# Optimization experiments

Measured on AMD Instinct MI355X. Metric: run time of the kernel, lower is better.

Reference implementation:

```python
import jax, jax.numpy as jnp
import numpy as np

EMBED_DIM = 1024
NUM_HEADS = 16
HEAD_DIM = EMBED_DIM // NUM_HEADS
BOARD = 32
SEQ = BOARD * BOARD
BATCH = 16


def setup_inputs() -> dict:
    key = jax.random.key(0)
    ks = jax.random.split(key, 6)
    x = jax.random.normal(ks[0], (BATCH, SEQ, EMBED_DIM), dtype=jnp.float32)
    scale = 1.0 / np.sqrt(EMBED_DIM)
    Wq = jax.random.normal(ks[1], (EMBED_DIM, EMBED_DIM), dtype=jnp.float32) * scale
    Wk = jax.random.normal(ks[2], (EMBED_DIM, EMBED_DIM), dtype=jnp.float32) * scale
    Wv = jax.random.normal(ks[3], (EMBED_DIM, EMBED_DIM), dtype=jnp.float32) * scale
    Wo = jax.random.normal(ks[4], (EMBED_DIM, EMBED_DIM), dtype=jnp.float32) * scale
    rel_bias = jax.random.normal(ks[5], (NUM_HEADS, 2 * BOARD - 1), dtype=jnp.float32)
    return {"x": x, "Wq": Wq, "Wk": Wk, "Wv": Wv, "Wo": Wo, "rel_bias": rel_bias}


def _rel_indices():
    # coords of the flattened H*W grid
    idx = jnp.arange(SEQ)
    rows = idx // BOARD
    cols = idx % BOARD
    offset = BOARD - 1
    rel_x = cols[None, :] - cols[:, None] + offset  # [S, S]
    rel_y = rows[None, :] - rows[:, None] + offset  # [S, S]
    return rel_x, rel_y


def reference(x, Wq, Wk, Wv, Wo, rel_bias):
    B, S, E = x.shape
    H, D = NUM_HEADS, HEAD_DIM
    # projections (Linear with bias=False: x @ W.T; weights here stored as [E, E] applied as x @ W)
    q = (x @ Wq).reshape(B, S, H, D).transpose(0, 2, 1, 3)  # [B,H,S,D]
    k = (x @ Wk).reshape(B, S, H, D).transpose(0, 2, 1, 3)
    v = (x @ Wv).reshape(B, S, H, D).transpose(0, 2, 1, 3)
    scores = jnp.einsum('bhqd,bhkd->bhqk', q, k) / jnp.sqrt(jnp.float32(D))
    rel_x, rel_y = _rel_indices()
    bias = rel_bias[:, rel_x] + rel_bias[:, rel_y]  # [H, S, S]
    scores = scores + bias[None]
    attn = jax.nn.softmax(scores, axis=-1)
    out = jnp.einsum('bhqk,bhkd->bhqd', attn, v)
    out = out.transpose(0, 2, 1, 3).reshape(B, S, E)
    return out @ Wo
```

## Files before the change

### kernel.cpp

```cpp
#include <hip/hip_runtime.h>

#define SEQ   1024
#define EMBED 1024
#define NH    16
#define HD    64
#define NB    16

typedef float facc4 __attribute__((ext_vector_type(4)));
typedef float facc16 __attribute__((ext_vector_type(16)));
typedef short frag8 __attribute__((ext_vector_type(8)));
typedef short sv4 __attribute__((ext_vector_type(4)));

__device__ __forceinline__ unsigned short f2bf(float f) {
  union { float f; unsigned int u; } c; c.f = f;
  unsigned int u = c.u;
  u += 0x7FFFu + ((u >> 16) & 1u);
  return (unsigned short)(u >> 16);
}

__device__ __forceinline__ unsigned int pk_bf16(float lo, float hi) {
  unsigned int r;
  asm("v_cvt_pk_bf16_f32 %0, %1, %2" : "=v"(r) : "v"(lo), "v"(hi));
  return r;
}

__device__ __forceinline__ void gl_lds16(const void* g, void* l) {
  __builtin_amdgcn_global_load_lds(
      (const __attribute__((address_space(1))) unsigned int*)g,
      (__attribute__((address_space(3))) unsigned int*)l, 16, 0, 0);
}

__global__ __launch_bounds__(256) void convert_x_kernel(
    const float* __restrict__ x, unsigned short* __restrict__ xb, int n8) {
  int stride = gridDim.x * blockDim.x;
  for (int i = blockIdx.x * blockDim.x + threadIdx.x; i < n8; i += stride) {
    const float4* src = (const float4*)(x + (size_t)i * 8);
    float4 v0 = src[0], v1 = src[1];
    frag8 o;
    o[0] = f2bf(v0.x); o[1] = f2bf(v0.y); o[2] = f2bf(v0.z); o[3] = f2bf(v0.w);
    o[4] = f2bf(v1.x); o[5] = f2bf(v1.y); o[6] = f2bf(v1.z); o[7] = f2bf(v1.w);
    *(frag8*)(xb + (size_t)i * 8) = o;
  }
}

__global__ __launch_bounds__(256) void transpose_w_kernel(
    const float* W0, const float* W1, const float* W2, const float* W3,
    unsigned short* T0, unsigned short* T1, unsigned short* T2, unsigned short* T3) {
  __shared__ float tw[64][65];
  const float* W; unsigned short* T;
  switch (blockIdx.z) {
    case 0: W = W0; T = T0; break;
    case 1: W = W1; T = T1; break;
    case 2: W = W2; T = T2; break;
    default: W = W3; T = T3; break;
  }
  int k0 = blockIdx.y * 64, n0 = blockIdx.x * 64;
  int t = threadIdx.x;
#pragma unroll
  for (int rep = 0; rep < 4; ++rep) {
    int c = rep * 256 + t;
    int row = c >> 4, ch = c & 15;
    float4 v = *(const float4*)(W + (size_t)(k0 + row) * 1024 + n0 + ch * 4);
    tw[row][ch * 4 + 0] = v.x; tw[row][ch * 4 + 1] = v.y;
    tw[row][ch * 4 + 2] = v.z; tw[row][ch * 4 + 3] = v.w;
  }
  __syncthreads();
#pragma unroll
  for (int rep = 0; rep < 2; ++rep) {
    int c = rep * 256 + t;
    int nrow = c >> 3, ch = c & 7;
    frag8 o;
#pragma unroll
    for (int i = 0; i < 8; ++i) o[i] = (short)f2bf(tw[ch * 8 + i][nrow]);
    *(frag8*)(T + (size_t)(n0 + nrow) * 1024 + k0 + ch * 8) = o;
  }
}

template <int MODE>
__global__ __launch_bounds__(512, 2) void gemm256(
    const unsigned short* __restrict__ A, const unsigned short* __restrict__ Bt,
    unsigned short* __restrict__ qo, unsigned short* __restrict__ ko,
    unsigned short* __restrict__ vto, float* __restrict__ fo, int N) {
  __shared__ unsigned short a_s[2][256 * 64];
  __shared__ unsigned short b_s[2][256 * 64];
  const int tid = threadIdx.x;
  const int w = tid >> 6, l = tid & 63;
  const int l15 = l & 15, l4 = l >> 4;
  const int wr = w >> 2, wc = w & 3;

  const int bid = blockIdx.x;
  const int xcd = bid & 7, j = bid >> 3;
  const int mt = xcd * 8 + (j & 7), nt = j >> 3;
  const int m0 = mt << 8, n0 = nt << 8;

  const int ldrow = l >> 3;
  const int swz8 = ((l & 7) ^ (ldrow & 7)) << 3;
  const unsigned short* Ab = A + (size_t)m0 * 1024;
  const unsigned short* Bb = Bt + (size_t)n0 * 1024;

  facc4 acc[8][4];
#pragma unroll
  for (int mi = 0; mi < 8; ++mi)
#pragma unroll
    for (int nj = 0; nj < 4; ++nj)
#pragma unroll
      for (int r = 0; r < 4; ++r) acc[mi][nj][r] = 0.f;

  auto STAGE = [&](int buf, int kt) {
#pragma unroll
    for (int i = 0; i < 4; ++i) {
      const int c = (w << 2) + i;
      gl_lds16(Ab + (size_t)kt * 64 + (size_t)((c << 3) + ldrow) * 1024 + swz8,
               &a_s[buf][c << 9]);
      gl_lds16(Bb + (size_t)kt * 64 + (size_t)((c << 3) + ldrow) * 1024 + swz8,
               &b_s[buf][c << 9]);
    }
  };

  STAGE(0, 0);
  STAGE(1, 1);
  asm volatile("s_waitcnt vmcnt(8)" ::: "memory");
  __builtin_amdgcn_s_barrier();
  __builtin_amdgcn_sched_barrier(0);

  const int rowA = (wr << 7) + l15;
  const int rowB = (wc << 6) + l15;

  for (int t = 0; t < 16; ++t) {
    const int cur = t & 1;
    const unsigned short* ap = a_s[cur];
    const unsigned short* bp = b_s[cur];
    frag8 af[8], bf[4];

#pragma unroll
    for (int mi = 0; mi < 8; ++mi) {
      const int r = rowA + (mi << 4);
      af[mi] = *(const frag8*)(ap + (r << 6) + ((l4 ^ (r & 7)) << 3));
    }
#pragma unroll
    for (int nj = 0; nj < 4; ++nj) {
      const int r = rowB + (nj << 4);
      bf[nj] = *(const frag8*)(bp + (r << 6) + ((l4 ^ (r & 7)) << 3));
    }
    __builtin_amdgcn_s_setprio(1);
#pragma unroll
    for (int mi = 0; mi < 8; ++mi)
#pragma unroll
      for (int nj = 0; nj < 4; ++nj)
        acc[mi][nj] = __builtin_amdgcn_mfma_f32_16x16x32_bf16(
            af[mi], bf[nj], acc[mi][nj], 0, 0, 0);
    __builtin_amdgcn_s_setprio(0);

    frag8 ag[8], bg[4];
#pragma unroll
    for (int mi = 0; mi < 8; ++mi) {
      const int r = rowA + (mi << 4);
      ag[mi] = *(const frag8*)(ap + (r << 6) + (((4 + l4) ^ (r & 7)) << 3));
    }
#pragma unroll
    for (int nj = 0; nj < 4; ++nj) {
      const int r = rowB + (nj << 4);
      bg[nj] = *(const frag8*)(bp + (r << 6) + (((4 + l4) ^ (r & 7)) << 3));
    }
    asm volatile("s_waitcnt lgkmcnt(0)" ::: "memory");
    __builtin_amdgcn_s_barrier();
    __builtin_amdgcn_sched_barrier(0);
    if (t + 2 < 16) STAGE(cur, t + 2);

    __builtin_amdgcn_s_setprio(1);
#pragma unroll
    for (int mi = 0; mi < 8; ++mi)
#pragma unroll
      for (int nj = 0; nj < 4; ++nj)
        acc[mi][nj] = __builtin_amdgcn_mfma_f32_16x16x32_bf16(
            ag[mi], bg[nj], acc[mi][nj], 0, 0, 0);
    __builtin_amdgcn_s_setprio(0);

    if (t < 14)       asm volatile("s_waitcnt vmcnt(8)" ::: "memory");
    else if (t == 14) asm volatile("s_waitcnt vmcnt(0)" ::: "memory");
    if (t < 15) {
      __builtin_amdgcn_s_barrier();
      __builtin_amdgcn_sched_barrier(0);
    }
  }

  const int m_base = m0 + (wr << 7);
  if (MODE == 0) {
    const int bb16 = (m_base >> 10) << 4;
#pragma unroll
    for (int nj = 0; nj < 4; ++nj) {
      const int n = n0 + (wc << 6) + (nj << 4) + l15;
      const int proj = n >> 10, rem = n & 1023;
      const int h = rem >> 6, d = rem & 63;
      const size_t bh16 = ((size_t)(bb16 + h)) << 16;
      if (proj == 2) {
#pragma unroll
        for (int mi = 0; mi < 8; ++mi) {
          const int s0 = (m_base + (mi << 4) + (l4 << 2)) & 1023;
          sv4 pv;
#pragma unroll
          for (int rr = 0; rr < 4; ++rr) pv[rr] = (short)f2bf(acc[mi][nj][rr]);
          *(sv4*)(vto + bh16 + ((size_t)d << 10) + s0) = pv;
        }
      } else {
        unsigned short* dst = (proj == 0) ? qo : ko;
#pragma unroll
        for (int mi = 0; mi < 8; ++mi)
#pragma unroll
          for (int rr = 0; rr < 4; ++rr) {
            const int s = (m_base + (mi << 4) + (l4 << 2) + rr) & 1023;
            dst[bh16 + (size_t)s * 64 + d] = f2bf(acc[mi][nj][rr]);
          }
      }
    }
  } else {
#pragma unroll
    for (int nj = 0; nj < 4; ++nj) {
      const int n = n0 + (wc << 6) + (nj << 4) + l15;
#pragma unroll
      for (int mi = 0; mi < 8; ++mi)
#pragma unroll
        for (int rr = 0; rr < 4; ++rr) {
          const int m = m_base + (mi << 4) + (l4 << 2) + rr;
          fo[(size_t)m * N + n] = acc[mi][nj][rr];
        }
    }
  }
}

__global__ __launch_bounds__(256, 4) void attn_kernel(
    const unsigned short* __restrict__ q, const unsigned short* __restrict__ k,
    const unsigned short* __restrict__ vt, const float* __restrict__ rel_bias,
    unsigned short* __restrict__ ao) {
  __shared__ unsigned short smem[16384];
  __shared__ float rb_s[63];
  unsigned short* k_s = smem;
  unsigned short* v_s = smem + 8192;

  const int bid = blockIdx.x;
  const int xcd = bid & 7, jj = bid >> 3;
  const int bh = xcd * 32 + (jj >> 3), qt = jj & 7;
  const int b = bh >> 4, h = bh & 15;
  const int t = threadIdx.x, w = t >> 6, l = t & 63;
  const int l31 = l & 31, hi = l >> 5;

  if (t < 63) rb_s[t] = rel_bias[h * 63 + t] * 1.44269504f;

  const unsigned short* qg = q + (size_t)bh * (SEQ * 64);
  const unsigned short* kg = k + (size_t)bh * (SEQ * 64);
  const unsigned short* vg = vt + (size_t)bh * (64 * SEQ);

  const int q0 = qt * 128 + w * 32;
  const int qr = q0 >> 5;

  frag8 qf[4];
#pragma unroll
  for (int s = 0; s < 4; ++s)
    qf[s] = *(const frag8*)(qg + (size_t)(q0 + l31) * 64 + s * 16 + hi * 8);

  auto STAGE = [&](int buf, int kt) {
#pragma unroll
    for (int i = 0; i < 2; ++i) {
      const int c = i * 256 + t;
      const int row = c >> 3, ch = c & 7;
      const int sw = (ch ^ (row & 7)) << 3;
      const int base = ((i * 256 + w * 64) << 3) + buf * 4096;
      gl_lds16(kg + (size_t)(kt * 64 + row) * 64 + sw, k_s + base);
      gl_lds16(vg + (size_t)row * SEQ + kt * 64 + sw, v_s + base);
    }
  };
  STAGE(0, 0);

  asm volatile("s_waitcnt lgkmcnt(0)" ::: "memory");
  __builtin_amdgcn_s_barrier();
  __builtin_amdgcn_sched_barrier(0);

  float bx[16];
#pragma unroll
  for (int r = 0; r < 16; ++r) {
    const int kc = (r & 3) + 8 * (r >> 2) + 4 * hi;
    bx[r] = rb_s[kc - l31 + 31];
  }

  float m_run = -1e30f, lsum = 0.f;
  facc16 o0, o1;
#pragma unroll
  for (int i = 0; i < 16; ++i) { o0[i] = 0.f; o1[i] = 0.f; }

  const float C1 = 0.125f * 1.44269504f;

  for (int kt = 0; kt < 16; ++kt) {
    const int p = kt & 1;
    if (kt < 15) {
      STAGE(p ^ 1, kt + 1);
      asm volatile("s_waitcnt vmcnt(4)" ::: "memory");
    } else {
      asm volatile("s_waitcnt vmcnt(0)" ::: "memory");
    }
    __builtin_amdgcn_s_barrier();
    __builtin_amdgcn_sched_barrier(0);

    const char* kp = (const char*)(k_s + p * 4096);
    const char* vp = (const char*)(v_s + p * 4096);

    facc16 sa[2];
    __builtin_amdgcn_s_setprio(1);
#pragma unroll
    for (int st = 0; st < 2; ++st) {
      facc16 z;
#pragma unroll
      for (int i = 0; i < 16; ++i) z[i] = 0.f;
#pragma unroll
      for (int s = 0; s < 4; ++s) {
        const int row = st * 32 + l31;
        const int byte_off = row * 128 + (((s * 2 + hi) ^ (row & 7)) << 4);
        frag8 kf = *(const frag8*)(kp + byte_off);
        z = __builtin_amdgcn_mfma_f32_32x32x16_bf16(kf, qf[s], z, 0, 0, 0);
      }
      sa[st] = z;
    }
    __builtin_amdgcn_s_setprio(0);

    const float by0 = rb_s[kt * 2 + 0 - qr + 31];
    const float by1 = rb_s[kt * 2 + 1 - qr + 31];
    float sc0[16], sc1[16];
#pragma unroll
    for (int r = 0; r < 16; ++r) {
      sc0[r] = __builtin_fmaf(sa[0][r], C1, bx[r]);
      sc1[r] = __builtin_fmaf(sa[1][r], C1, bx[r]);
    }
    float m0 = sc0[0], m1 = sc1[0];
#pragma unroll
    for (int r = 1; r < 16; ++r) { m0 = fmaxf(m0, sc0[r]); m1 = fmaxf(m1, sc1[r]); }
    float tm = fmaxf(m0 + by0, m1 + by1);
    tm = fmaxf(tm, __shfl_xor(tm, 32));
    if (!__all(tm <= m_run + 8.f)) {
      const float mn = fmaxf(m_run, tm);
      const float corr = __builtin_amdgcn_exp2f(m_run - mn);
      lsum *= corr;
#pragma unroll
      for (int i = 0; i < 16; ++i) { o0[i] *= corr; o1[i] *= corr; }
      m_run = mn;
    }
    const float mb0 = m_run - by0, mb1 = m_run - by1;
    float p0[16], p1[16];
    float ps = 0.f;
#pragma unroll
    for (int r = 0; r < 16; ++r) {
      p0[r] = __builtin_amdgcn_exp2f(sc0[r] - mb0);
      p1[r] = __builtin_amdgcn_exp2f(sc1[r] - mb1);
      ps += p0[r] + p1[r];
    }
    ps += __shfl_xor(ps, 32);
    lsum += ps;

    unsigned int fw[4][4];
#pragma unroll
    for (int ks = 0; ks < 4; ++ks) {
      const float* pp = (ks < 2) ? p0 : p1;
      const int R0 = (ks & 1) * 8;
      const int R1 = R0 + 4;
      const unsigned int w00 = pk_bf16(pp[R0 + 0], pp[R0 + 1]);
      const unsigned int w01 = pk_bf16(pp[R0 + 2], pp[R0 + 3]);
      const unsigned int w10 = pk_bf16(pp[R1 + 0], pp[R1 + 1]);
      const unsigned int w11 = pk_bf16(pp[R1 + 2], pp[R1 + 3]);
      const unsigned int s0 = hi ? w00 : w10;
      const unsigned int s1 = hi ? w01 : w11;
      const unsigned int r0 = __shfl_xor((int)s0, 32);
      const unsigned int r1 = __shfl_xor((int)s1, 32);
      fw[ks][0] = hi ? r0 : w00;
      fw[ks][1] = hi ? r1 : w01;
      fw[ks][2] = hi ? w10 : r0;
      fw[ks][3] = hi ? w11 : r1;
    }

    __builtin_amdgcn_s_setprio(1);
#pragma unroll
    for (int ks = 0; ks < 4; ++ks) {
      frag8 pb;
      {
        union { unsigned int u[4]; frag8 f; } cv;
        cv.u[0] = fw[ks][0]; cv.u[1] = fw[ks][1];
        cv.u[2] = fw[ks][2]; cv.u[3] = fw[ks][3];
        pb = cv.f;
      }
      {
        const int row = l31;
        const int byte_off = row * 128 + (((ks * 2 + hi) ^ (row & 7)) << 4);
        frag8 vf = *(const frag8*)(vp + byte_off);
        o0 = __builtin_amdgcn_mfma_f32_32x32x16_bf16(vf, pb, o0, 0, 0, 0);
      }
      {
        const int row = 32 + l31;
        const int byte_off = row * 128 + (((ks * 2 + hi) ^ (row & 7)) << 4);
        frag8 vf = *(const frag8*)(vp + byte_off);
        o1 = __builtin_amdgcn_mfma_f32_32x32x16_bf16(vf, pb, o1, 0, 0, 0);
      }
    }
    __builtin_amdgcn_s_setprio(0);

    asm volatile("s_waitcnt lgkmcnt(0)" ::: "memory");
    __builtin_amdgcn_s_barrier();
    __builtin_amdgcn_sched_barrier(0);
  }

  const float inv = __builtin_amdgcn_rcpf(lsum);
  unsigned short (*os)[72] = (unsigned short (*)[72])(smem + w * (32 * 72));
#pragma unroll
  for (int dt = 0; dt < 2; ++dt) {
#pragma unroll
    for (int r = 0; r < 16; r += 2) {
      const int d = (r & 3) + 8 * (r >> 2) + 4 * hi + 32 * dt;
      const float e0 = (dt ? o1[r] : o0[r]) * inv;
      const float e1 = (dt ? o1[r + 1] : o0[r + 1]) * inv;
      *(unsigned int*)&os[l31][d] = pk_bf16(e0, e1);
    }
  }
  asm volatile("s_waitcnt lgkmcnt(0)" ::: "memory");
  __builtin_amdgcn_sched_barrier(0);
#pragma unroll
  for (int i = 0; i < 4; ++i) {
    const int c = i * 64 + l;
    const int qrow = c >> 3, ch = c & 7;
    frag8 ov = *(const frag8*)(&os[qrow][ch * 8]);
    *(frag8*)(ao + ((size_t)(b * SEQ + q0 + qrow) * EMBED + h * 64 + ch * 8)) = ov;
  }
}

extern "C" void kernel_launch(void* const* d_in, const int* in_sizes, int n_in,
                              void* d_out, int out_size, void* d_ws, size_t ws_size,
                              hipStream_t stream) {
  (void)in_sizes; (void)n_in; (void)out_size; (void)ws_size;
  const float* x  = (const float*)d_in[0];
  const float* Wq = (const float*)d_in[1];
  const float* Wk = (const float*)d_in[2];
  const float* Wv = (const float*)d_in[3];
  const float* Wo = (const float*)d_in[4];
  const float* rb = (const float*)d_in[5];
  float* out = (float*)d_out;

  unsigned short* xb  = (unsigned short*)d_ws;
  unsigned short* wtq = xb + 16777216;
  unsigned short* wtk = wtq + 1048576;
  unsigned short* wtv = wtk + 1048576;
  unsigned short* wto = wtv + 1048576;
  unsigned short* qb  = wto + 1048576;
  unsigned short* kb  = qb + 16777216;
  unsigned short* aob = kb + 16777216;
  unsigned short* vtb = aob + 16777216;

  convert_x_kernel<<<4096, 256, 0, stream>>>(x, xb, 16777216 / 8);
  transpose_w_kernel<<<dim3(16, 16, 4), 256, 0, stream>>>(
      Wq, Wk, Wv, Wo, wtq, wtk, wtv, wto);
  gemm256<0><<<768, 512, 0, stream>>>(
      xb, wtq, qb, kb, vtb, nullptr, 3072);
  attn_kernel<<<2048, 256, 0, stream>>>(qb, kb, vtb, rb, aob);
  gemm256<1><<<256, 512, 0, stream>>>(
      aob, wto, nullptr, nullptr, nullptr, out, 1024);
}
```

Before: 272.2 us.

## Restructure GEMM main loop into four-quadrant ping-pong schedule with split A/B staging

Reorganizes the projection GEMM inner loop so each K-step is processed as four 64x32 quadrant MFMA clusters that reuse A and B fragments in a snake order. Global-to-LDS staging is split into A and B halves: A is prefetched one step ahead and B two steps ahead, interleaved between the clusters. The aim is to overlap global loads and LDS reads with MFMA work more finely and to lower register pressure from fragment arrays. It adds more barriers per iteration and carries a risk of LDS hazards given the tighter buffer reuse.

```diff
diff --git a/kernel.cpp b/kernel.cpp
--- a/kernel.cpp
+++ b/kernel.cpp
@@ -106,79 +106,134 @@
 #pragma unroll
       for (int r = 0; r < 4; ++r) acc[mi][nj][r] = 0.f;
 
-  auto STAGE = [&](int buf, int kt) {
-#pragma unroll
-    for (int i = 0; i < 4; ++i) {
-      const int c = (w << 2) + i;
-      gl_lds16(Ab + (size_t)kt * 64 + (size_t)((c << 3) + ldrow) * 1024 + swz8,
-               &a_s[buf][c << 9]);
-      gl_lds16(Bb + (size_t)kt * 64 + (size_t)((c << 3) + ldrow) * 1024 + swz8,
-               &b_s[buf][c << 9]);
+  auto STAGE_A = [&](int buf, int half, int kt) {
+#pragma unroll
+    for (int i = 0; i < 2; ++i) {
+      const int c = (w << 1) + i;
+      const int rb = (half << 7) + (c << 3);
+      gl_lds16(Ab + (size_t)kt * 64 + (size_t)(rb + ldrow) * 1024 + swz8,
+               &a_s[buf][rb << 6]);
     }
   };
-
-  STAGE(0, 0);
-  STAGE(1, 1);
-  asm volatile("s_waitcnt vmcnt(8)" ::: "memory");
+  auto STAGE_B = [&](int buf, int half, int kt) {
+#pragma unroll
+    for (int i = 0; i < 2; ++i) {
+      const int c = (w << 1) + i;
+      const int rb = (half << 7) + (c << 3);
+      gl_lds16(Bb + (size_t)kt * 64 + (size_t)(rb + ldrow) * 1024 + swz8,
+               &b_s[buf][rb << 6]);
+    }
+  };
+
+  STAGE_A(0, 0, 0); STAGE_A(0, 1, 0);
+  STAGE_B(0, 0, 0); STAGE_B(0, 1, 0);
+  STAGE_B(1, 0, 1); STAGE_B(1, 1, 1);
+  asm volatile("s_waitcnt vmcnt(4)" ::: "memory");
   __builtin_amdgcn_s_barrier();
   __builtin_amdgcn_sched_barrier(0);
 
   const int rowA = (wr << 7) + l15;
   const int rowB = (wc << 6) + l15;
 
-  for (int t = 0; t < 16; ++t) {
-    const int cur = t & 1;
-    const unsigned short* ap = a_s[cur];
-    const unsigned short* bp = b_s[cur];
-    frag8 af[8], bf[4];
-
-#pragma unroll
-    for (int mi = 0; mi < 8; ++mi) {
+  frag8 aq[4][2], bq0[2][2], bq1[2][2];
+
+  for (int u = 0; u < 16; ++u) {
+    const int p = u & 1;
+    const unsigned short* ap = a_s[p];
+    const unsigned short* bp = b_s[p];
+
+#pragma unroll
+    for (int mi = 0; mi < 4; ++mi) {
       const int r = rowA + (mi << 4);
-      af[mi] = *(const frag8*)(ap + (r << 6) + ((l4 ^ (r & 7)) << 3));
-    }
-#pragma unroll
-    for (int nj = 0; nj < 4; ++nj) {
+#pragma unroll
+      for (int ks = 0; ks < 2; ++ks)
+        aq[mi][ks] = *(const frag8*)(ap + (r << 6) + ((((ks << 2) | l4) ^ (r & 7)) << 3));
+    }
+#pragma unroll
+    for (int nj = 0; nj < 2; ++nj) {
       const int r = rowB + (nj << 4);
-      bf[nj] = *(const frag8*)(bp + (r << 6) + ((l4 ^ (r & 7)) << 3));
-    }
+#pragma unroll
+      for (int ks = 0; ks < 2; ++ks)
+        bq0[nj][ks] = *(const frag8*)(bp + (r << 6) + ((((ks << 2) | l4) ^ (r & 7)) << 3));
+    }
+    if (u + 1 < 16) STAGE_A(p ^ 1, 0, u + 1);
+    asm volatile("s_waitcnt lgkmcnt(8)" ::: "memory");
+    __builtin_amdgcn_s_barrier();
+    asm volatile("s_waitcnt lgkmcnt(0)" ::: "memory");
+    __builtin_amdgcn_sched_barrier(0);
     __builtin_amdgcn_s_setprio(1);
 #pragma unroll
-    for (int mi = 0; mi < 8; ++mi)
-#pragma unroll
-      for (int nj = 0; nj < 4; ++nj)
-        acc[mi][nj] = __builtin_amdgcn_mfma_f32_16x16x32_bf16(
-            af[mi], bf[nj], acc[mi][nj], 0, 0, 0);
+    for (int ks = 0; ks < 2; ++ks)
+#pragma unroll
+      for (int mi = 0; mi < 4; ++mi)
+#pragma unroll
+        for (int nj = 0; nj < 2; ++nj)
+          acc[mi][nj] = __builtin_amdgcn_mfma_f32_16x16x32_bf16(
+              aq[mi][ks], bq0[nj][ks], acc[mi][nj], 0, 0, 0);
     __builtin_amdgcn_s_setprio(0);
-
-    frag8 ag[8], bg[4];
-#pragma unroll
-    for (int mi = 0; mi < 8; ++mi) {
-      const int r = rowA + (mi << 4);
-      ag[mi] = *(const frag8*)(ap + (r << 6) + (((4 + l4) ^ (r & 7)) << 3));
-    }
-#pragma unroll
-    for (int nj = 0; nj < 4; ++nj) {
-      const int r = rowB + (nj << 4);
-      bg[nj] = *(const frag8*)(bp + (r << 6) + (((4 + l4) ^ (r & 7)) << 3));
-    }
+    __builtin_amdgcn_s_barrier();
+
+#pragma unroll
+    for (int nj = 0; nj < 2; ++nj) {
+      const int r = rowB + ((nj + 2) << 4);
+#pragma unroll
+      for (int ks = 0; ks < 2; ++ks)
+        bq1[nj][ks] = *(const frag8*)(bp + (r << 6) + ((((ks << 2) | l4) ^ (r & 7)) << 3));
+    }
+    if (u + 1 < 16) STAGE_A(p ^ 1, 1, u + 1);
+    __builtin_amdgcn_s_barrier();
     asm volatile("s_waitcnt lgkmcnt(0)" ::: "memory");
-    __builtin_amdgcn_s_barrier();
     __builtin_amdgcn_sched_barrier(0);
-    if (t + 2 < 16) STAGE(cur, t + 2);
-
     __builtin_amdgcn_s_setprio(1);
 #pragma unroll
-    for (int mi = 0; mi < 8; ++mi)
-#pragma unroll
-      for (int nj = 0; nj < 4; ++nj)
-        acc[mi][nj] = __builtin_amdgcn_mfma_f32_16x16x32_bf16(
-            ag[mi], bg[nj], acc[mi][nj], 0, 0, 0);
+    for (int ks = 0; ks < 2; ++ks)
+#pragma unroll
+      for (int mi = 0; mi < 4; ++mi)
+#pragma unroll
+        for (int nj = 0; nj < 2; ++nj)
+          acc[mi][nj + 2] = __builtin_amdgcn_mfma_f32_16x16x32_bf16(
+              aq[mi][ks], bq1[nj][ks], acc[mi][nj + 2], 0, 0, 0);
     __builtin_amdgcn_s_setprio(0);
-
-    if (t < 14)       asm volatile("s_waitcnt vmcnt(8)" ::: "memory");
-    else if (t == 14) asm volatile("s_waitcnt vmcnt(0)" ::: "memory");
-    if (t < 15) {
+    __builtin_amdgcn_s_barrier();
+
+#pragma unroll
+    for (int mi = 0; mi < 4; ++mi) {
+      const int r = rowA + ((mi + 4) << 4);
+#pragma unroll
+      for (int ks = 0; ks < 2; ++ks)
+        aq[mi][ks] = *(const frag8*)(ap + (r << 6) + ((((ks << 2) | l4) ^ (r & 7)) << 3));
+    }
+    if (u + 2 < 16) STAGE_B(p, 0, u + 2);
+    __builtin_amdgcn_s_barrier();
+    asm volatile("s_waitcnt lgkmcnt(0)" ::: "memory");
+    __builtin_amdgcn_sched_barrier(0);
+    __builtin_amdgcn_s_setprio(1);
+#pragma unroll
+    for (int ks = 0; ks < 2; ++ks)
+#pragma unroll
+      for (int mi = 0; mi < 4; ++mi)
+#pragma unroll
+        for (int nj = 0; nj < 2; ++nj)
+          acc[mi + 4][nj + 2] = __builtin_amdgcn_mfma_f32_16x16x32_bf16(
+              aq[mi][ks], bq1[nj][ks], acc[mi + 4][nj + 2], 0, 0, 0);
+    __builtin_amdgcn_s_setprio(0);
+    __builtin_amdgcn_s_barrier();
+
+    if (u + 2 < 16) STAGE_B(p, 1, u + 2);
+    __builtin_amdgcn_s_barrier();
+    __builtin_amdgcn_s_setprio(1);
+#pragma unroll
+    for (int ks = 0; ks < 2; ++ks)
+#pragma unroll
+      for (int mi = 0; mi < 4; ++mi)
+#pragma unroll
+        for (int nj = 0; nj < 2; ++nj)
+          acc[mi + 4][nj] = __builtin_amdgcn_mfma_f32_16x16x32_bf16(
+              aq[mi][ks], bq0[nj][ks], acc[mi + 4][nj], 0, 0, 0);
+    __builtin_amdgcn_s_setprio(0);
+    if (u < 14)       asm volatile("s_waitcnt vmcnt(4)" ::: "memory");
+    else if (u == 14) asm volatile("s_waitcnt vmcnt(0)" ::: "memory");
+    if (u < 15) {
       __builtin_amdgcn_s_barrier();
       __builtin_amdgcn_sched_barrier(0);
     }
```

Result: slower. 287.0 us (+5.4%).
